# Performance work log

Hardware: AMD Instinct MI355X
Metric: run time of the kernel (lower is better)

The kernel has to match this reference:

```python
import jax, jax.numpy as jnp
import numpy as np

N_NODES = 16384
N_EDGES = 8192
D_FEAT = 64


def setup_inputs() -> dict:
    key = jax.random.key(0)
    k1, k2 = jax.random.split(key)
    incidence_matrix = jax.random.uniform(k1, (N_NODES, N_EDGES), dtype=jnp.float32)
    features = jax.random.normal(k2, (N_NODES, D_FEAT), dtype=jnp.float32)
    return {"incidence_matrix": incidence_matrix, "features": features}


def reference(incidence_matrix, features):
    # Faithful to the original: compute_degree_matrices returns RAW degree
    # diagonals (no inversion despite variable names). torch.diag(d) @ X is
    # exactly a row-broadcast scaling d[:, None] * X.
    d_v = jnp.sum(incidence_matrix, axis=1)  # [N] node degrees
    d_e = jnp.sum(incidence_matrix, axis=0)  # [M] hyperedge degrees
    X = features * d_v[:, None]                       # D_v @ X        [N, d]
    X_hyperedge = incidence_matrix.T @ X              # H^T @ X        [M, d]
    X_hyperedge = X_hyperedge * d_e[:, None]          # D_e @ (.)      [M, d]
    X = incidence_matrix @ X_hyperedge                # H @ (.)        [N, d]
    X = X * d_v[:, None]                              # D_v @ (.)      [N, d]
    return X
```

## Files before the change

### kernel.cpp

```cpp
#include <hip/hip_runtime.h>

#define N_NODES 16384
#define N_EDGES 8192
#define D_FEAT  64

typedef __attribute__((ext_vector_type(8))) short short8;
typedef __attribute__((ext_vector_type(4))) float floatx4;

__device__ __forceinline__ unsigned short f2bf(float f) {
    unsigned int u = __float_as_uint(f);
    return (unsigned short)((u + 0x7fffu + ((u >> 16) & 1u)) >> 16);
}

__device__ __forceinline__ int sw(int row, int g) {
    return row * 32 + (g ^ (((row >> 3) & 7) * 4));
}

__global__ __launch_bounds__(256) void dvscale_kernel(const float* __restrict__ H,
                                                      const float* __restrict__ F,
                                                      float* __restrict__ dv,
                                                      unsigned short* __restrict__ Hbf,
                                                      float* __restrict__ Xs) {
    const int wave = threadIdx.x >> 6;
    const int lane = threadIdx.x & 63;
    const int n = blockIdx.x * 4 + wave;
    const float4* row = (const float4*)(H + (size_t)n * N_EDGES);
    unsigned short* hrow = Hbf + (size_t)n * N_EDGES;
    float s = 0.f;
#pragma unroll
    for (int j = 0; j < 32; ++j) {
        float4 v = row[lane + 64 * j];
        s += v.x + v.y + v.z + v.w;
        unsigned long long pk = (unsigned long long)f2bf(v.x)
                              | ((unsigned long long)f2bf(v.y) << 16)
                              | ((unsigned long long)f2bf(v.z) << 32)
                              | ((unsigned long long)f2bf(v.w) << 48);
        *(unsigned long long*)(hrow + 4 * (lane + 64 * j)) = pk;
    }
#pragma unroll
    for (int off = 32; off > 0; off >>= 1) s += __shfl_down(s, off, 64);
    s = __shfl(s, 0, 64);
    if (lane == 0) dv[n] = s;
    Xs[(size_t)n * D_FEAT + lane] = F[(size_t)n * D_FEAT + lane] * s;
}

__global__ __launch_bounds__(256) void xst_kernel(const float* __restrict__ Xs,
                                                  unsigned short* __restrict__ XsT) {
    __shared__ float tile[64][65];
    const int n0 = blockIdx.x * 64;
    const int t = threadIdx.x;
    const int r = t >> 4, c4 = t & 15;
#pragma unroll
    for (int li = 0; li < 4; ++li) {
        const int rr = r + 16 * li;
        float4 v = *(const float4*)(Xs + (size_t)(n0 + rr) * 64 + c4 * 4);
        tile[rr][c4 * 4 + 0] = v.x; tile[rr][c4 * 4 + 1] = v.y;
        tile[rr][c4 * 4 + 2] = v.z; tile[rr][c4 * 4 + 3] = v.w;
    }
    __syncthreads();
#pragma unroll
    for (int li = 0; li < 4; ++li) {
        const int d = r + 16 * li;
        unsigned long long pk = (unsigned long long)f2bf(tile[c4 * 4 + 0][d])
                              | ((unsigned long long)f2bf(tile[c4 * 4 + 1][d]) << 16)
                              | ((unsigned long long)f2bf(tile[c4 * 4 + 2][d]) << 32)
                              | ((unsigned long long)f2bf(tile[c4 * 4 + 3][d]) << 48);
        *(unsigned long long*)(XsT + (size_t)d * N_NODES + n0 + c4 * 4) = pk;
    }
}

__global__ __launch_bounds__(256) void gemm1_kernel(const unsigned short* __restrict__ Hbf,
                                                    const unsigned short* __restrict__ XsT,
                                                    float* __restrict__ YaccT,
                                                    float* __restrict__ de) {
    __shared__ unsigned int A32[128 * 32];
    __shared__ unsigned int B32[64 * 32];
    const int t = threadIdx.x;
    const int w = t >> 6;
    const int lane = t & 63;
    const int e0 = (blockIdx.x & 63) * 128;
    const int k0base = (blockIdx.x >> 6) * 1024;

    const int seg = t & 15;
    const int p = t >> 4;
    const int bd = t >> 3;
    const int bseg = t & 7;

    floatx4 acc[2][4];
#pragma unroll
    for (int i = 0; i < 2; ++i)
#pragma unroll
        for (int j = 0; j < 4; ++j) acc[i][j] = (floatx4){0.f, 0.f, 0.f, 0.f};
    float dea[8] = {0.f, 0.f, 0.f, 0.f, 0.f, 0.f, 0.f, 0.f};

    for (int it = 0; it < 16; ++it) {
        const int k0 = k0base + it * 64;
        __syncthreads();
#pragma unroll
        for (int pp = 0; pp < 2; ++pp) {
            const int pr = p + 16 * pp;
            const unsigned short* src = Hbf + (size_t)(k0 + 2 * pr) * N_EDGES + e0 + seg * 8;
            short8 r0 = *(const short8*)src;
            short8 r1 = *(const short8*)(src + N_EDGES);
#pragma unroll
            for (int j = 0; j < 8; ++j) {
                unsigned int lo = (unsigned short)r0[j];
                unsigned int hi = (unsigned short)r1[j];
                unsigned int pk = lo | (hi << 16);
                const int e = seg * 8 + j;
                A32[sw(e, pr & ~3) + (pr & 3)] = pk;
                dea[j] += __uint_as_float(pk << 16) + __uint_as_float(pk & 0xffff0000u);
            }
        }
#pragma unroll
        for (int bb = 0; bb < 2; ++bb) {
            const int d = bd + 32 * bb;
            uint4 v = *(const uint4*)(XsT + (size_t)d * N_NODES + k0 + bseg * 8);
            *(uint4*)&B32[sw(d, bseg * 4)] = v;
        }
        __syncthreads();
#pragma unroll
        for (int s = 0; s < 2; ++s) {
            const int g = s * 16 + (lane >> 4) * 4;
            short8 af[2];
#pragma unroll
            for (int i = 0; i < 2; ++i) {
                const int row = 32 * w + 16 * i + (lane & 15);
                af[i] = *(short8*)&A32[sw(row, g)];
            }
#pragma unroll
            for (int j = 0; j < 4; ++j) {
                const int row = 16 * j + (lane & 15);
                short8 bf = *(short8*)&B32[sw(row, g)];
#pragma unroll
                for (int i = 0; i < 2; ++i)
                    acc[i][j] = __builtin_amdgcn_mfma_f32_16x16x32_bf16(af[i], bf, acc[i][j], 0, 0, 0);
            }
        }
    }

#pragma unroll
    for (int i = 0; i < 2; ++i)
#pragma unroll
        for (int j = 0; j < 4; ++j)
#pragma unroll
            for (int r = 0; r < 4; ++r) {
                const int e = e0 + 32 * w + 16 * i + (lane >> 4) * 4 + r;
                const int d = 16 * j + (lane & 15);
                atomicAdd(&YaccT[(size_t)d * N_EDGES + e], acc[i][j][r]);
            }
#pragma unroll
    for (int j = 0; j < 8; ++j) atomicAdd(&de[e0 + seg * 8 + j], dea[j]);
}

__global__ __launch_bounds__(256) void scaley_kernel(const float* __restrict__ YaccT,
                                                     const float* __restrict__ de,
                                                     unsigned short* __restrict__ Yt) {
    const int idx = blockIdx.x * 256 + threadIdx.x;
    const int d = idx >> 11;
    const int e4 = idx & 2047;
    float4 y = ((const float4*)YaccT)[idx];
    float4 sc = ((const float4*)de)[e4];
    unsigned long long pk = (unsigned long long)f2bf(y.x * sc.x)
                          | ((unsigned long long)f2bf(y.y * sc.y) << 16)
                          | ((unsigned long long)f2bf(y.z * sc.z) << 32)
                          | ((unsigned long long)f2bf(y.w * sc.w) << 48);
    *(unsigned long long*)(Yt + (size_t)d * N_EDGES + e4 * 4) = pk;
}

__global__ __launch_bounds__(256) void gemm2_kernel(const unsigned short* __restrict__ Hbf,
                                                    const unsigned short* __restrict__ Yt,
                                                    float* __restrict__ OutAcc) {
    __shared__ unsigned int A32[128 * 32];
    __shared__ unsigned int B32[64 * 32];
    const int t = threadIdx.x;
    const int w = t >> 6;
    const int lane = t & 63;
    const int m0 = (blockIdx.x & 127) * 128;
    const int k0base = (blockIdx.x >> 7) * 1024;

    const int aseg = t & 7;
    const int am = t >> 3;
    const int bd = t >> 3;
    const int bseg = t & 7;

    floatx4 acc[2][4];
#pragma unroll
    for (int i = 0; i < 2; ++i)
#pragma unroll
        for (int j = 0; j < 4; ++j) acc[i][j] = (floatx4){0.f, 0.f, 0.f, 0.f};

    for (int it = 0; it < 16; ++it) {
        const int k0 = k0base + it * 64;
        __syncthreads();
#pragma unroll
        for (int li = 0; li < 4; ++li) {
            const int m = am + 32 * li;
            uint4 v = *(const uint4*)(Hbf + (size_t)(m0 + m) * N_EDGES + k0 + aseg * 8);
            *(uint4*)&A32[sw(m, aseg * 4)] = v;
        }
#pragma unroll
        for (int bb = 0; bb < 2; ++bb) {
            const int d = bd + 32 * bb;
            uint4 v = *(const uint4*)(Yt + (size_t)d * N_EDGES + k0 + bseg * 8);
            *(uint4*)&B32[sw(d, bseg * 4)] = v;
        }
        __syncthreads();
#pragma unroll
        for (int s = 0; s < 2; ++s) {
            const int g = s * 16 + (lane >> 4) * 4;
            short8 af[2];
#pragma unroll
            for (int i = 0; i < 2; ++i) {
                const int row = 32 * w + 16 * i + (lane & 15);
                af[i] = *(short8*)&A32[sw(row, g)];
            }
#pragma unroll
            for (int j = 0; j < 4; ++j) {
                const int row = 16 * j + (lane & 15);
                short8 bf = *(short8*)&B32[sw(row, g)];
#pragma unroll
                for (int i = 0; i < 2; ++i)
                    acc[i][j] = __builtin_amdgcn_mfma_f32_16x16x32_bf16(af[i], bf, acc[i][j], 0, 0, 0);
            }
        }
    }

#pragma unroll
    for (int i = 0; i < 2; ++i)
#pragma unroll
        for (int j = 0; j < 4; ++j)
#pragma unroll
            for (int r = 0; r < 4; ++r) {
                const int n = m0 + 32 * w + 16 * i + (lane >> 4) * 4 + r;
                const int d = 16 * j + (lane & 15);
                atomicAdd(&OutAcc[(size_t)n * D_FEAT + d], acc[i][j][r]);
            }
}

__global__ __launch_bounds__(256) void scaleout_kernel(const float* __restrict__ OutAcc,
                                                       const float* __restrict__ dv,
                                                       float* __restrict__ out) {
    const int idx = blockIdx.x * 256 + threadIdx.x;
    const int n = idx >> 4;
    const float d = dv[n];
    float4 v = ((const float4*)OutAcc)[idx];
    v.x *= d; v.y *= d; v.z *= d; v.w *= d;
    ((float4*)out)[idx] = v;
}

extern "C" void kernel_launch(void* const* d_in, const int* in_sizes, int n_in,
                              void* d_out, int out_size, void* d_ws, size_t ws_size,
                              hipStream_t stream) {
    const float* H = (const float*)d_in[0];
    const float* F = (const float*)d_in[1];
    float* out = (float*)d_out;
    char* base = (char*)d_ws;

    float* dv = (float*)base;
    float* de = (float*)(base + 65536);
    float* Xs = (float*)(base + 98304);
    float* YaccT = (float*)(base + 98304 + 4194304);
    float* OutAcc = (float*)(base + 98304 + 4194304 + 2097152);
    unsigned short* XsT = (unsigned short*)(base + 98304 + 4194304 + 2097152 + 4194304);
    unsigned short* Yt = XsT + (size_t)64 * N_NODES;
    unsigned short* Hbf = (unsigned short*)((char*)Yt + 1048576);

    hipMemsetAsync(de, 0, N_EDGES * sizeof(float), stream);
    hipMemsetAsync(YaccT, 0, (size_t)64 * N_EDGES * sizeof(float), stream);
    hipMemsetAsync(OutAcc, 0, (size_t)N_NODES * D_FEAT * sizeof(float), stream);

    dvscale_kernel<<<N_NODES / 4, 256, 0, stream>>>(H, F, dv, Hbf, Xs);
    xst_kernel<<<N_NODES / 64, 256, 0, stream>>>(Xs, XsT);
    gemm1_kernel<<<1024, 256, 0, stream>>>(Hbf, XsT, YaccT, de);
    scaley_kernel<<<512, 256, 0, stream>>>(YaccT, de, Yt);
    gemm2_kernel<<<1024, 256, 0, stream>>>(Hbf, Yt, OutAcc);
    scaleout_kernel<<<1024, 256, 0, stream>>>(OutAcc, dv, out);
}
```

Before: 1.005 ms.

## Drop split-K atomics in gemm2, double-buffer LDS, fuse output scaling, speed bf16 conversion

gemm2 now gives each block 64 full rows and walks the whole K range itself. It uses double-buffered LDS with register prefetch, so the atomic accumulation buffer, its memset and the separate scaleout kernel all go away, and the dv scaling is applied directly in the epilogue. The dvscale kernel converts floats to bf16 with the hardware packed-convert instruction, uses non-temporal loads and writes 16-byte stores. The trade-off is that only 256 blocks run, each with a long 128-iteration serial K loop, which may underfill the GPU's compute units.

```diff
diff --git a/kernel.cpp b/kernel.cpp
--- a/kernel.cpp
+++ b/kernel.cpp
@@ -10,6 +10,12 @@
 __device__ __forceinline__ unsigned short f2bf(float f) {
     unsigned int u = __float_as_uint(f);
     return (unsigned short)((u + 0x7fffu + ((u >> 16) & 1u)) >> 16);
+}
+
+__device__ __forceinline__ unsigned int cvtpk(float lo, float hi) {
+    unsigned int r;
+    asm("v_cvt_pk_bf16_f32 %0, %1, %2" : "=v"(r) : "v"(lo), "v"(hi));
+    return r;
 }
 
 __device__ __forceinline__ int sw(int row, int g) {
@@ -24,18 +30,21 @@
     const int wave = threadIdx.x >> 6;
     const int lane = threadIdx.x & 63;
     const int n = blockIdx.x * 4 + wave;
-    const float4* row = (const float4*)(H + (size_t)n * N_EDGES);
+    const floatx4* row = (const floatx4*)(H + (size_t)n * N_EDGES);
     unsigned short* hrow = Hbf + (size_t)n * N_EDGES;
     float s = 0.f;
 #pragma unroll
-    for (int j = 0; j < 32; ++j) {
-        float4 v = row[lane + 64 * j];
-        s += v.x + v.y + v.z + v.w;
-        unsigned long long pk = (unsigned long long)f2bf(v.x)
-                              | ((unsigned long long)f2bf(v.y) << 16)
-                              | ((unsigned long long)f2bf(v.z) << 32)
-                              | ((unsigned long long)f2bf(v.w) << 48);
-        *(unsigned long long*)(hrow + 4 * (lane + 64 * j)) = pk;
+    for (int j = 0; j < 16; ++j) {
+        floatx4 v0 = __builtin_nontemporal_load(&row[2 * lane + 128 * j]);
+        floatx4 v1 = __builtin_nontemporal_load(&row[2 * lane + 128 * j + 1]);
+        s += v0[0] + v0[1] + v0[2] + v0[3];
+        s += v1[0] + v1[1] + v1[2] + v1[3];
+        uint4 pk;
+        pk.x = cvtpk(v0[0], v0[1]);
+        pk.y = cvtpk(v0[2], v0[3]);
+        pk.z = cvtpk(v1[0], v1[1]);
+        pk.w = cvtpk(v1[2], v1[3]);
+        *(uint4*)(hrow + 8 * (lane + 64 * j)) = pk;
     }
 #pragma unroll
     for (int off = 32; off > 0; off >>= 1) s += __shfl_down(s, off, 64);
@@ -166,87 +175,89 @@
                           | ((unsigned long long)f2bf(y.z * sc.z) << 32)
                           | ((unsigned long long)f2bf(y.w * sc.w) << 48);
     *(unsigned long long*)(Yt + (size_t)d * N_EDGES + e4 * 4) = pk;
+    (void)d;
 }
 
 __global__ __launch_bounds__(256) void gemm2_kernel(const unsigned short* __restrict__ Hbf,
                                                     const unsigned short* __restrict__ Yt,
-                                                    float* __restrict__ OutAcc) {
-    __shared__ unsigned int A32[128 * 32];
-    __shared__ unsigned int B32[64 * 32];
+                                                    const float* __restrict__ dv,
+                                                    float* __restrict__ out) {
+    __shared__ unsigned int A32[2][64 * 32];
+    __shared__ unsigned int B32[2][64 * 32];
     const int t = threadIdx.x;
     const int w = t >> 6;
     const int lane = t & 63;
-    const int m0 = (blockIdx.x & 127) * 128;
-    const int k0base = (blockIdx.x >> 7) * 1024;
-
+    const int m0 = blockIdx.x * 64;
+
+    const int arow = t >> 3;
     const int aseg = t & 7;
-    const int am = t >> 3;
-    const int bd = t >> 3;
-    const int bseg = t & 7;
-
-    floatx4 acc[2][4];
-#pragma unroll
-    for (int i = 0; i < 2; ++i)
-#pragma unroll
-        for (int j = 0; j < 4; ++j) acc[i][j] = (floatx4){0.f, 0.f, 0.f, 0.f};
-
-    for (int it = 0; it < 16; ++it) {
-        const int k0 = k0base + it * 64;
+
+    const int l15 = lane & 15;
+    const int l4 = lane >> 4;
+
+    floatx4 acc[4];
+#pragma unroll
+    for (int j = 0; j < 4; ++j) acc[j] = (floatx4){0.f, 0.f, 0.f, 0.f};
+
+    uint4 ra0, ra1, rb0, rb1;
+
+    const unsigned short* aptr0 = Hbf + (size_t)(m0 + arow) * N_EDGES + aseg * 8;
+    const unsigned short* aptr1 = Hbf + (size_t)(m0 + arow + 32) * N_EDGES + aseg * 8;
+    const unsigned short* bptr0 = Yt + (size_t)arow * N_EDGES + aseg * 8;
+    const unsigned short* bptr1 = Yt + (size_t)(arow + 32) * N_EDGES + aseg * 8;
+
+#define G2_LOAD(k0)                                     \
+    do {                                                \
+        ra0 = *(const uint4*)(aptr0 + (k0));            \
+        ra1 = *(const uint4*)(aptr1 + (k0));            \
+        rb0 = *(const uint4*)(bptr0 + (k0));            \
+        rb1 = *(const uint4*)(bptr1 + (k0));            \
+    } while (0)
+
+#define G2_WRITE(buf)                                   \
+    do {                                                \
+        *(uint4*)&A32[buf][sw(arow, aseg * 4)] = ra0;   \
+        *(uint4*)&A32[buf][sw(arow + 32, aseg * 4)] = ra1; \
+        *(uint4*)&B32[buf][sw(arow, aseg * 4)] = rb0;   \
+        *(uint4*)&B32[buf][sw(arow + 32, aseg * 4)] = rb1; \
+    } while (0)
+
+    G2_LOAD(0);
+    G2_WRITE(0);
+    G2_LOAD(64);
+    __syncthreads();
+
+    int cur = 0;
+    for (int it = 0; it < 128; ++it) {
+        if (it < 127) G2_WRITE(cur ^ 1);
+        if (it < 126) G2_LOAD((it + 2) * 64);
+#pragma unroll
+        for (int s = 0; s < 2; ++s) {
+            const int g = s * 16 + l4 * 4;
+            short8 af = *(short8*)&A32[cur][sw(16 * w + l15, g)];
+#pragma unroll
+            for (int j = 0; j < 4; ++j) {
+                short8 bfv = *(short8*)&B32[cur][sw(16 * j + l15, g)];
+                acc[j] = __builtin_amdgcn_mfma_f32_16x16x32_bf16(af, bfv, acc[j], 0, 0, 0);
+            }
+        }
         __syncthreads();
-#pragma unroll
-        for (int li = 0; li < 4; ++li) {
-            const int m = am + 32 * li;
-            uint4 v = *(const uint4*)(Hbf + (size_t)(m0 + m) * N_EDGES + k0 + aseg * 8);
-            *(uint4*)&A32[sw(m, aseg * 4)] = v;
-        }
-#pragma unroll
-        for (int bb = 0; bb < 2; ++bb) {
-            const int d = bd + 32 * bb;
-            uint4 v = *(const uint4*)(Yt + (size_t)d * N_EDGES + k0 + bseg * 8);
-            *(uint4*)&B32[sw(d, bseg * 4)] = v;
-        }
-        __syncthreads();
-#pragma unroll
-        for (int s = 0; s < 2; ++s) {
-            const int g = s * 16 + (lane >> 4) * 4;
-            short8 af[2];
-#pragma unroll
-            for (int i = 0; i < 2; ++i) {
-                const int row = 32 * w + 16 * i + (lane & 15);
-                af[i] = *(short8*)&A32[sw(row, g)];
-            }
-#pragma unroll
-            for (int j = 0; j < 4; ++j) {
-                const int row = 16 * j + (lane & 15);
-                short8 bf = *(short8*)&B32[sw(row, g)];
-#pragma unroll
-                for (int i = 0; i < 2; ++i)
-                    acc[i][j] = __builtin_amdgcn_mfma_f32_16x16x32_bf16(af[i], bf, acc[i][j], 0, 0, 0);
-            }
-        }
-    }
-
-#pragma unroll
-    for (int i = 0; i < 2; ++i)
-#pragma unroll
-        for (int j = 0; j < 4; ++j)
-#pragma unroll
-            for (int r = 0; r < 4; ++r) {
-                const int n = m0 + 32 * w + 16 * i + (lane >> 4) * 4 + r;
-                const int d = 16 * j + (lane & 15);
-                atomicAdd(&OutAcc[(size_t)n * D_FEAT + d], acc[i][j][r]);
-            }
-}
-
-__global__ __launch_bounds__(256) void scaleout_kernel(const float* __restrict__ OutAcc,
-                                                       const float* __restrict__ dv,
-                                                       float* __restrict__ out) {
-    const int idx = blockIdx.x * 256 + threadIdx.x;
-    const int n = idx >> 4;
-    const float d = dv[n];
-    float4 v = ((const float4*)OutAcc)[idx];
-    v.x *= d; v.y *= d; v.z *= d; v.w *= d;
-    ((float4*)out)[idx] = v;
+        cur ^= 1;
+    }
+
+    float dvv[4];
+#pragma unroll
+    for (int r = 0; r < 4; ++r) dvv[r] = dv[m0 + 16 * w + l4 * 4 + r];
+#pragma unroll
+    for (int j = 0; j < 4; ++j)
+#pragma unroll
+        for (int r = 0; r < 4; ++r) {
+            const int n = m0 + 16 * w + l4 * 4 + r;
+            const int d = 16 * j + l15;
+            out[(size_t)n * D_FEAT + d] = acc[j][r] * dvv[r];
+        }
+#undef G2_LOAD
+#undef G2_WRITE
 }
 
 extern "C" void kernel_launch(void* const* d_in, const int* in_sizes, int n_in,
@@ -261,19 +272,16 @@
     float* de = (float*)(base + 65536);
     float* Xs = (float*)(base + 98304);
     float* YaccT = (float*)(base + 98304 + 4194304);
-    float* OutAcc = (float*)(base + 98304 + 4194304 + 2097152);
     unsigned short* XsT = (unsigned short*)(base + 98304 + 4194304 + 2097152 + 4194304);
     unsigned short* Yt = XsT + (size_t)64 * N_NODES;
     unsigned short* Hbf = (unsigned short*)((char*)Yt + 1048576);
 
-    hipMemsetAsync(de, 0, N_EDGES * sizeof(float), stream);
-    hipMemsetAsync(YaccT, 0, (size_t)64 * N_EDGES * sizeof(float), stream);
-    hipMemsetAsync(OutAcc, 0, (size_t)N_NODES * D_FEAT * sizeof(float), stream);
+    (void)hipMemsetAsync(de, 0, N_EDGES * sizeof(float), stream);
+    (void)hipMemsetAsync(YaccT, 0, (size_t)64 * N_EDGES * sizeof(float), stream);
 
     dvscale_kernel<<<N_NODES / 4, 256, 0, stream>>>(H, F, dv, Hbf, Xs);
     xst_kernel<<<N_NODES / 64, 256, 0, stream>>>(Xs, XsT);
     gemm1_kernel<<<1024, 256, 0, stream>>>(Hbf, XsT, YaccT, de);
     scaley_kernel<<<512, 256, 0, stream>>>(YaccT, de, Yt);
-    gemm2_kernel<<<1024, 256, 0, stream>>>(Hbf, Yt, OutAcc);
-    scaleout_kernel<<<1024, 256, 0, stream>>>(OutAcc, dv, out);
-}
+    gemm2_kernel<<<256, 256, 0, stream>>>(Hbf, Yt, dv, out);
+}
```

After: 1.029 ms. 1.02x slower.
